# Kernel tuning notes

Measured on AMD Instinct MI355X. Metric: run time of the kernel, lower is better.

## Reference

```python
import jax, jax.numpy as jnp
import numpy as np

D_HIDDEN = 1024
N_HEADS = 16
D_HEAD = 64
B, N = 4, 1024
EPS = 1e-5


def _lin(x, w, b):
    # torch Linear: y = x @ W^T + b, w: [out, in]
    return jnp.einsum('...i,oi->...o', x, w) + b


def _ln(x, g, b):
    m = jnp.mean(x, axis=-1, keepdims=True)
    v = jnp.mean(jnp.square(x - m), axis=-1, keepdims=True)
    return (x - m) * jax.lax.rsqrt(v + EPS) * g + b


def setup_inputs() -> dict:
    key = jax.random.key(0)
    ks = jax.random.split(key, 20)
    d = D_HIDDEN
    s = 0.02
    inp = {
        'x': jax.random.normal(ks[0], (B, N, d), jnp.float32),
        'time_emb': jax.random.normal(ks[1], (B, d), jnp.float32),
        'ln1_g': jnp.ones((d,), jnp.float32),
        'ln1_b': jnp.zeros((d,), jnp.float32),
        's1_w': jax.random.normal(ks[2], (d, d), jnp.float32) * s,
        's1_b': jnp.zeros((d,), jnp.float32),
        'o1_w': jax.random.normal(ks[3], (d, d), jnp.float32) * s,
        'o1_b': jnp.zeros((d,), jnp.float32),
        'qkv_w': jax.random.normal(ks[4], (3 * d, d), jnp.float32) * s,
        'qkv_b': jnp.zeros((3 * d,), jnp.float32),
        'proj_w': jax.random.normal(ks[5], (d, d), jnp.float32) * s,
        'proj_b': jnp.zeros((d,), jnp.float32),
        'ln2_g': jnp.ones((d,), jnp.float32),
        'ln2_b': jnp.zeros((d,), jnp.float32),
        's2_w': jax.random.normal(ks[6], (d, d), jnp.float32) * s,
        's2_b': jnp.zeros((d,), jnp.float32),
        'o2_w': jax.random.normal(ks[7], (d, d), jnp.float32) * s,
        'o2_b': jnp.zeros((d,), jnp.float32),
        'up_w': jax.random.normal(ks[8], (4 * d, d), jnp.float32) * s,
        'up_b': jnp.zeros((4 * d,), jnp.float32),
        'down_w': jax.random.normal(ks[9], (d, 4 * d), jnp.float32) * s,
        'down_b': jnp.zeros((d,), jnp.float32),
    }
    return inp


def reference(x, time_emb, ln1_g, ln1_b, s1_w, s1_b, o1_w, o1_b,
              qkv_w, qkv_b, proj_w, proj_b, ln2_g, ln2_b,
              s2_w, s2_b, o2_w, o2_b, up_w, up_b, down_w, down_b):
    d = D_HIDDEN

    def ada(h, sw, sb, ow, ob):
        scale = _lin(time_emb, sw, sb)[:, None, :]   # [B,1,d]
        offset = _lin(time_emb, ow, ob)[:, None, :]
        return (1.0 + scale) * h + offset

    # attention branch
    h = ada(_ln(x, ln1_g, ln1_b), s1_w, s1_b, o1_w, o1_b)
    qkv = _lin(h, qkv_w, qkv_b)                       # [B,N,3d]
    q, k, v = jnp.split(qkv, 3, axis=-1)
    q = q.reshape(B, N, N_HEADS, D_HEAD)
    k = k.reshape(B, N, N_HEADS, D_HEAD)
    v = v.reshape(B, N, N_HEADS, D_HEAD)
    wei = jnp.einsum('bnhd,bmhd->bhnm', q, k) * (D_HEAD ** -0.5)
    wei = jax.nn.softmax(wei, axis=-1)
    attn = jnp.einsum('bhnm,bmhd->bnhd', wei, v).reshape(B, N, d)
    x = x + _lin(attn, proj_w, proj_b)

    # mlp branch (torch nn.GELU default = exact erf gelu)
    h = ada(_ln(x, ln2_g, ln2_b), s2_w, s2_b, o2_w, o2_b)
    h = jax.nn.gelu(_lin(h, up_w, up_b), approximate=False)
    x = x + _lin(h, down_w, down_b)
    return x, time_emb
```

## Files before the change

kernel.cpp:

```cpp
#include <hip/hip_runtime.h>
#include <hip/hip_bf16.h>
#include <math.h>

#define DH 1024
#define BB 4
#define NN 1024
#define NH 16
#define HD 64

typedef __attribute__((ext_vector_type(8))) short bf16x8;
typedef __attribute__((ext_vector_type(4))) float f32x4;
typedef unsigned short u16;

static __device__ __forceinline__ u16 f2bf(float f) {
  __hip_bfloat16 h = __float2bfloat16(f);
  return *reinterpret_cast<u16*>(&h);
}

#define MFMA16(a, b, c) __builtin_amdgcn_mfma_f32_16x16x32_bf16(a, b, c, 0, 0, 0)
#define VMCNT(n) asm volatile("s_waitcnt vmcnt(" #n ")" ::: "memory")
#define MEMFENCE asm volatile("" ::: "memory")

static __device__ __forceinline__ void async16(const void* g, void* l) {
  __builtin_amdgcn_global_load_lds(
      (const __attribute__((address_space(1))) void*)g,
      (__attribute__((address_space(3))) void*)l, 16, 0, 0);
}

__global__ void cvt_bf16_kernel(const float* __restrict__ in, u16* __restrict__ out, int n4) {
  int i = blockIdx.x * blockDim.x + threadIdx.x;
  if (i >= n4) return;
  float4 v = reinterpret_cast<const float4*>(in)[i];
  ushort4 o;
  o.x = f2bf(v.x); o.y = f2bf(v.y); o.z = f2bf(v.z); o.w = f2bf(v.w);
  reinterpret_cast<ushort4*>(out)[i] = o;
}

__global__ __launch_bounds__(256) void adaln_kernel(
    const float* __restrict__ e,
    const float* __restrict__ w_s1, const float* __restrict__ b_s1,
    const float* __restrict__ w_o1, const float* __restrict__ b_o1,
    const float* __restrict__ w_s2, const float* __restrict__ b_s2,
    const float* __restrict__ w_o2, const float* __restrict__ b_o2,
    float* __restrict__ out) {
  int tid = threadIdx.x, wid = tid >> 6, lane = tid & 63;
  int mat = blockIdx.y;
  const float* w; const float* bs; float addc;
  if (mat == 0)      { w = w_s1; bs = b_s1; addc = 1.f; }
  else if (mat == 1) { w = w_o1; bs = b_o1; addc = 0.f; }
  else if (mat == 2) { w = w_s2; bs = b_s2; addc = 1.f; }
  else               { w = w_o2; bs = b_o2; addc = 0.f; }
  int col = blockIdx.x * 4 + wid;
  float a0 = 0.f, a1 = 0.f, a2 = 0.f, a3 = 0.f;
  const float* wc_ = w + (size_t)col * DH;
  for (int i = 0; i < 16; ++i) {
    int k = i * 64 + lane;
    float wv = wc_[k];
    a0 += wv * e[k];
    a1 += wv * e[DH + k];
    a2 += wv * e[2 * DH + k];
    a3 += wv * e[3 * DH + k];
  }
  #pragma unroll
  for (int msk = 32; msk; msk >>= 1) {
    a0 += __shfl_xor(a0, msk); a1 += __shfl_xor(a1, msk);
    a2 += __shfl_xor(a2, msk); a3 += __shfl_xor(a3, msk);
  }
  if (lane == 0) {
    float bb = bs[col] + addc;
    out[mat * (4 * DH) + 0 * DH + col] = a0 + bb;
    out[mat * (4 * DH) + 1 * DH + col] = a1 + bb;
    out[mat * (4 * DH) + 2 * DH + col] = a2 + bb;
    out[mat * (4 * DH) + 3 * DH + col] = a3 + bb;
  }
}

__global__ __launch_bounds__(256) void ln_mod_kernel(
    const float* __restrict__ x, const float* __restrict__ g, const float* __restrict__ bta,
    const float* __restrict__ sp, const float* __restrict__ off, u16* __restrict__ out) {
  int row = blockIdx.x;
  int b = row >> 10;
  int tid = threadIdx.x;
  int wid = tid >> 6, lane = tid & 63;
  const float4 xv = reinterpret_cast<const float4*>(x + (size_t)row * DH)[tid];
  float s = xv.x + xv.y + xv.z + xv.w;
  float ss = xv.x * xv.x + xv.y * xv.y + xv.z * xv.z + xv.w * xv.w;
  #pragma unroll
  for (int m = 32; m; m >>= 1) { s += __shfl_xor(s, m); ss += __shfl_xor(ss, m); }
  __shared__ float red[8];
  if (lane == 0) { red[wid] = s; red[4 + wid] = ss; }
  __syncthreads();
  s = red[0] + red[1] + red[2] + red[3];
  ss = red[4] + red[5] + red[6] + red[7];
  float mean = s * (1.f / DH);
  float var = ss * (1.f / DH) - mean * mean;
  float rstd = rsqrtf(var + 1e-5f);
  int c = tid * 4;
  const float* spb = sp + b * DH + c;
  const float* offb = off + b * DH + c;
  float y0 = (xv.x - mean) * rstd * g[c + 0] + bta[c + 0];
  float y1 = (xv.y - mean) * rstd * g[c + 1] + bta[c + 1];
  float y2 = (xv.z - mean) * rstd * g[c + 2] + bta[c + 2];
  float y3 = (xv.w - mean) * rstd * g[c + 3] + bta[c + 3];
  ushort4 o;
  o.x = f2bf(spb[0] * y0 + offb[0]);
  o.y = f2bf(spb[1] * y1 + offb[1]);
  o.z = f2bf(spb[2] * y2 + offb[2]);
  o.w = f2bf(spb[3] * y3 + offb[3]);
  reinterpret_cast<ushort4*>(out + (size_t)row * DH)[tid] = o;
}

enum { EPI_BF16 = 0, EPI_GELU = 1, EPI_F32PART = 2 };

template <int EPI>
__global__ __launch_bounds__(512, 2) void gemm256_kernel(
    const u16* __restrict__ A, const u16* __restrict__ W,
    const float* __restrict__ bias, void* __restrict__ outp,
    int N, int K, int KT) {
  extern __shared__ u16 lds[];
  u16* Ab = lds;
  u16* Bb = lds + 32768;
  int tid = threadIdx.x;
  int wid = tid >> 6, lane = tid & 63;
  int l15 = lane & 15, l4 = lane >> 4;
  int wr = wid >> 2, wc = wid & 3;

  int nwg = gridDim.x * gridDim.y;
  int lin = blockIdx.y * gridDim.x + blockIdx.x;
  int q8 = nwg >> 3;
  int lin2 = (lin & 7) * q8 + (lin >> 3);
  int bx = lin2 % gridDim.x, by = lin2 / gridDim.x;
  int m0 = by * 256, n0 = bx * 256;
  int k0 = blockIdx.z * (KT << 5);

  f32x4 acc[8][4] = {};

  const u16* Abase = A + (size_t)m0 * K + k0;
  const u16* Wbase = W + (size_t)n0 * K + k0;
  int i0 = tid, i1 = 512 + tid;
  int r0 = i0 >> 2, c0 = (i0 & 3) ^ ((r0 >> 1) & 3);
  int r1 = i1 >> 2, c1 = (i1 & 3) ^ ((r1 >> 1) & 3);
  size_t gO0 = (size_t)r0 * K + c0 * 8;
  size_t gO1 = (size_t)r1 * K + c1 * 8;
  int lb0 = (wid * 64) * 8;
  int lb1 = (512 + wid * 64) * 8;

  auto stage = [&](int tt) {
    int q = (tt & 3) * 8192;
    const u16* Ak = Abase + tt * 32;
    const u16* Wk = Wbase + tt * 32;
    async16(Ak + gO0, &Ab[q + lb0]);
    async16(Ak + gO1, &Ab[q + lb1]);
    async16(Wk + gO0, &Bb[q + lb0]);
    async16(Wk + gO1, &Bb[q + lb1]);
  };

  auto compute = [&](int tt) {
    int q = (tt & 3) * 8192;
    bf16x8 af[8], bfr[4];
    #pragma unroll
    for (int m = 0; m < 8; ++m) {
      int row = wr * 128 + m * 16 + l15;
      int ps = l4 ^ ((row >> 1) & 3);
      af[m] = *reinterpret_cast<const bf16x8*>(&Ab[q + row * 32 + ps * 8]);
    }
    #pragma unroll
    for (int n = 0; n < 4; ++n) {
      int row = wc * 64 + n * 16 + l15;
      int ps = l4 ^ ((row >> 1) & 3);
      bfr[n] = *reinterpret_cast<const bf16x8*>(&Bb[q + row * 32 + ps * 8]);
    }
    #pragma unroll
    for (int m = 0; m < 8; ++m)
      #pragma unroll
      for (int n = 0; n < 4; ++n)
        acc[m][n] = MFMA16(af[m], bfr[n], acc[m][n]);
  };

  stage(0);
  if (KT > 1) stage(1);
  if (KT > 2) stage(2);
  for (int t = 0; t < KT; ++t) {
    if (t < KT - 3) { stage(t + 3); VMCNT(12); }
    else if (t == KT - 3) { VMCNT(8); }
    else if (t == KT - 2) { VMCNT(4); }
    else { VMCNT(0); }
    __builtin_amdgcn_s_barrier();
    MEMFENCE;
    compute(t);
    MEMFENCE;
    __builtin_amdgcn_s_barrier();
  }

  int M = gridDim.y * 256;
  float* fout = (float*)outp + (size_t)blockIdx.z * M * N;
  #pragma unroll
  for (int n = 0; n < 4; ++n) {
    int col = n0 + wc * 64 + n * 16 + l15;
    float bv = (EPI == EPI_F32PART) ? 0.f : bias[col];
    #pragma unroll
    for (int m = 0; m < 8; ++m) {
      #pragma unroll
      for (int r = 0; r < 4; ++r) {
        int rowg = m0 + wr * 128 + m * 16 + l4 * 4 + r;
        float v = acc[m][n][r] + bv;
        if (EPI == EPI_GELU) {
          v = 0.5f * v * (1.f + erff(v * 0.70710678118f));
          ((u16*)outp)[(size_t)rowg * N + col] = f2bf(v);
        } else if (EPI == EPI_BF16) {
          ((u16*)outp)[(size_t)rowg * N + col] = f2bf(v);
        } else {
          fout[(size_t)rowg * N + col] = v;
        }
      }
    }
  }
}

enum { OEPI_BF16 = 0, OEPI_GELU = 1, OEPI_RES = 2 };

template <int EPI>
__global__ __launch_bounds__(256, 3) void gemm_bt_kernel(
    const u16* __restrict__ A, const u16* __restrict__ W,
    const float* __restrict__ bias, const float* __restrict__ resid,
    void* __restrict__ outp, int N, int K) {
  __shared__ __align__(16) u16 As[2][128 * 32];
  __shared__ __align__(16) u16 Ws[2][128 * 32];
  int tid = threadIdx.x;
  int wid = tid >> 6, lane = tid & 63;
  int l15 = lane & 15, l4 = lane >> 4;
  int m0 = blockIdx.y * 128, n0 = blockIdx.x * 128;
  int wr = wid >> 1, wc = wid & 1;
  f32x4 acc[4][4] = {};

  const int KT = K >> 5;
  int idx0 = tid, idx1 = 256 + tid;
  int rowA0 = idx0 >> 2, gs0 = (idx0 & 3) ^ ((rowA0 >> 1) & 3);
  int rowA1 = idx1 >> 2, gs1 = (idx1 & 3) ^ ((rowA1 >> 1) & 3);
  const u16* Abase = A + (size_t)m0 * K;
  const u16* Wbase = W + (size_t)n0 * K;
  int lb0 = (wid * 64) * 8;
  int lb1 = (256 + wid * 64) * 8;

  auto stage = [&](int buf, int kt) {
    const u16* Ak = Abase + kt * 32;
    const u16* Wk = Wbase + kt * 32;
    async16(Ak + (size_t)rowA0 * K + gs0 * 8, &As[buf][lb0]);
    async16(Wk + (size_t)rowA0 * K + gs0 * 8, &Ws[buf][lb0]);
    async16(Ak + (size_t)rowA1 * K + gs1 * 8, &As[buf][lb1]);
    async16(Wk + (size_t)rowA1 * K + gs1 * 8, &Ws[buf][lb1]);
  };

  auto compute = [&](int buf) {
    bf16x8 af[4], wf[4];
    #pragma unroll
    for (int m = 0; m < 4; ++m) {
      int row = wr * 64 + m * 16 + l15;
      int ps = l4 ^ ((row >> 1) & 3);
      af[m] = *reinterpret_cast<const bf16x8*>(&As[buf][row * 32 + ps * 8]);
    }
    #pragma unroll
    for (int n = 0; n < 4; ++n) {
      int row = wc * 64 + n * 16 + l15;
      int ps = l4 ^ ((row >> 1) & 3);
      wf[n] = *reinterpret_cast<const bf16x8*>(&Ws[buf][row * 32 + ps * 8]);
    }
    #pragma unroll
    for (int m = 0; m < 4; ++m)
      #pragma unroll
      for (int n = 0; n < 4; ++n)
        acc[m][n] = MFMA16(af[m], wf[n], acc[m][n]);
  };

  stage(0, 0);
  __syncthreads();
  int buf = 0;
  for (int kt = 0; kt < KT - 1; ++kt) {
    stage(buf ^ 1, kt + 1);
    compute(buf);
    __syncthreads();
    buf ^= 1;
  }
  compute(buf);

  #pragma unroll
  for (int n = 0; n < 4; ++n) {
    int col = n0 + wc * 64 + n * 16 + l15;
    float bv = bias[col];
    #pragma unroll
    for (int m = 0; m < 4; ++m) {
      #pragma unroll
      for (int r = 0; r < 4; ++r) {
        int rowg = m0 + wr * 64 + m * 16 + l4 * 4 + r;
        float v = acc[m][n][r] + bv;
        if (EPI == OEPI_GELU) {
          v = 0.5f * v * (1.f + erff(v * 0.70710678118f));
          ((u16*)outp)[(size_t)rowg * N + col] = f2bf(v);
        } else if (EPI == OEPI_BF16) {
          ((u16*)outp)[(size_t)rowg * N + col] = f2bf(v);
        } else {
          ((float*)outp)[(size_t)rowg * N + col] = v + resid[(size_t)rowg * N + col];
        }
      }
    }
  }
}

__global__ __launch_bounds__(256) void reduce4_kernel(
    const float* __restrict__ part, const float* __restrict__ x2,
    const float* __restrict__ bias, float* __restrict__ out) {
  size_t i = (size_t)blockIdx.x * 256 + threadIdx.x;
  const size_t MN4 = (size_t)4096 * 1024 / 4;
  float4 a0 = reinterpret_cast<const float4*>(part)[i];
  float4 a1 = reinterpret_cast<const float4*>(part)[i + MN4];
  float4 a2 = reinterpret_cast<const float4*>(part)[i + 2 * MN4];
  float4 a3 = reinterpret_cast<const float4*>(part)[i + 3 * MN4];
  float4 xr = reinterpret_cast<const float4*>(x2)[i];
  int col = (int)((i * 4) & 1023);
  float4 bv = *reinterpret_cast<const float4*>(&bias[col]);
  float4 o;
  o.x = xr.x + bv.x + a0.x + a1.x + a2.x + a3.x;
  o.y = xr.y + bv.y + a0.y + a1.y + a2.y + a3.y;
  o.z = xr.z + bv.z + a0.z + a1.z + a2.z + a3.z;
  o.w = xr.w + bv.w + a0.w + a1.w + a2.w + a3.w;
  reinterpret_cast<float4*>(out)[i] = o;
}

__global__ __launch_bounds__(256, 4) void attn_kernel(
    const u16* __restrict__ qkv, u16* __restrict__ out) {
  __shared__ __align__(16) u16 Ks[64 * 64];
  __shared__ __align__(16) u16 Vt[64 * 64];
  __shared__ __align__(16) u16 Ps[4][16 * 64];
  int tid = threadIdx.x, wid = tid >> 6, lane = tid & 63;
  int l15 = lane & 15, l4 = lane >> 4;
  int qt = blockIdx.x, bh = blockIdx.y;
  int b = bh >> 4, h = bh & 15;
  const size_t SN = 3 * DH;
  const u16* qb = qkv + (size_t)b * NN * SN + h * HD;
  const u16* kb = qb + DH;
  const u16* vb = qb + 2 * DH;

  int qrow = qt * 64 + wid * 16 + l15;
  bf16x8 qf[2];
  #pragma unroll
  for (int ks = 0; ks < 2; ++ks)
    qf[ks] = *reinterpret_cast<const bf16x8*>(qb + (size_t)qrow * SN + ks * 32 + l4 * 8);

  float m_[4], l_[4];
  f32x4 o_[4] = {};
  #pragma unroll
  for (int r = 0; r < 4; ++r) { m_[r] = -1e30f; l_[r] = 0.f; }

  int idxA = tid, idxB = 256 + tid;
  int jA = idxA >> 3, sA = idxA & 7, gsA = sA ^ (jA & 7);
  int jB = idxB >> 3, sB = idxB & 7, gsB = sB ^ (jB & 7);
  int lbA = (wid * 64) * 8;
  int lbB = (256 + wid * 64) * 8;

  for (int t = 0; t < 16; ++t) {
    __syncthreads();
    const u16* ktb = kb + (size_t)t * 64 * SN;
    async16(ktb + (size_t)jA * SN + gsA * 8, &Ks[lbA]);
    async16(ktb + (size_t)jB * SN + gsB * 8, &Ks[lbB]);
    const u16* vtb = vb + (size_t)t * 64 * SN;
    {
      bf16x8 v0 = *reinterpret_cast<const bf16x8*>(vtb + (size_t)jA * SN + sA * 8);
      bf16x8 v1 = *reinterpret_cast<const bf16x8*>(vtb + (size_t)jB * SN + sB * 8);
      #pragma unroll
      for (int e = 0; e < 8; ++e) {
        int d = sA * 8 + e;
        int ps = (jA >> 3) ^ (d & 7) ^ ((d >> 3) & 7);
        Vt[d * 64 + ps * 8 + (jA & 7)] = v0[e];
        int d2 = sB * 8 + e;
        int ps2 = (jB >> 3) ^ (d2 & 7) ^ ((d2 >> 3) & 7);
        Vt[d2 * 64 + ps2 * 8 + (jB & 7)] = v1[e];
      }
    }
    __syncthreads();

    f32x4 sa[4];
    #pragma unroll
    for (int nb = 0; nb < 4; ++nb) {
      f32x4 s = {};
      #pragma unroll
      for (int ks = 0; ks < 2; ++ks) {
        int j = nb * 16 + l15;
        int ps = (ks * 4 + l4) ^ (j & 7);
        bf16x8 kf = *reinterpret_cast<const bf16x8*>(&Ks[j * 64 + ps * 8]);
        s = MFMA16(qf[ks], kf, s);
      }
      sa[nb] = s * 0.125f;
    }

    float corr[4], tsum[4];
    #pragma unroll
    for (int r = 0; r < 4; ++r) {
      float v = fmaxf(fmaxf(sa[0][r], sa[1][r]), fmaxf(sa[2][r], sa[3][r]));
      #pragma unroll
      for (int msk = 1; msk < 16; msk <<= 1) v = fmaxf(v, __shfl_xor(v, msk));
      float mn = fmaxf(m_[r], v);
      corr[r] = __expf(m_[r] - mn);
      m_[r] = mn;
      tsum[r] = 0.f;
    }
    #pragma unroll
    for (int nb = 0; nb < 4; ++nb) {
      #pragma unroll
      for (int r = 0; r < 4; ++r) {
        float p = __expf(sa[nb][r] - m_[r]);
        sa[nb][r] = p;
        tsum[r] += p;
      }
    }
    #pragma unroll
    for (int r = 0; r < 4; ++r) {
      float v = tsum[r];
      #pragma unroll
      for (int msk = 1; msk < 16; msk <<= 1) v += __shfl_xor(v, msk);
      l_[r] = l_[r] * corr[r] + v;
    }
    #pragma unroll
    for (int nd = 0; nd < 4; ++nd) {
      #pragma unroll
      for (int r = 0; r < 4; ++r) o_[nd][r] *= corr[r];
    }

    u16* Pw = Ps[wid];
    #pragma unroll
    for (int nb = 0; nb < 4; ++nb) {
      int slot = nb * 2 + (l15 >> 3);
      #pragma unroll
      for (int r = 0; r < 4; ++r) {
        int row = l4 * 4 + r;
        int ps = slot ^ (row & 7);
        Pw[row * 64 + ps * 8 + (l15 & 7)] = f2bf(sa[nb][r]);
      }
    }
    #pragma unroll
    for (int ks = 0; ks < 2; ++ks) {
      int psp = (ks * 4 + l4) ^ (l15 & 7);
      bf16x8 pa = *reinterpret_cast<const bf16x8*>(&Pw[l15 * 64 + psp * 8]);
      #pragma unroll
      for (int nd = 0; nd < 4; ++nd) {
        int d = nd * 16 + l15;
        int psv = (ks * 4 + l4) ^ (d & 7) ^ ((d >> 3) & 7);
        bf16x8 vf = *reinterpret_cast<const bf16x8*>(&Vt[d * 64 + psv * 8]);
        o_[nd] = MFMA16(pa, vf, o_[nd]);
      }
    }
  }

  float inv[4];
  #pragma unroll
  for (int r = 0; r < 4; ++r) inv[r] = 1.f / l_[r];
  u16* ob = out + (size_t)b * NN * DH + h * HD;
  #pragma unroll
  for (int nd = 0; nd < 4; ++nd) {
    #pragma unroll
    for (int r = 0; r < 4; ++r) {
      int q = qt * 64 + wid * 16 + l4 * 4 + r;
      ob[(size_t)q * DH + nd * 16 + l15] = f2bf(o_[nd][r] * inv[r]);
    }
  }
}

__global__ void copy_te_kernel(const float* __restrict__ te, float* __restrict__ out) {
  int i = blockIdx.x * blockDim.x + threadIdx.x;
  if (i < BB * DH) out[i] = te[i];
}

extern "C" void kernel_launch(void* const* d_in, const int* in_sizes, int n_in,
                              void* d_out, int out_size, void* d_ws, size_t ws_size,
                              hipStream_t stream) {
  (void)in_sizes; (void)n_in; (void)out_size; (void)ws_size;
  const float* x      = (const float*)d_in[0];
  const float* te     = (const float*)d_in[1];
  const float* ln1_g  = (const float*)d_in[2];
  const float* ln1_b  = (const float*)d_in[3];
  const float* s1_w   = (const float*)d_in[4];
  const float* s1_b   = (const float*)d_in[5];
  const float* o1_w   = (const float*)d_in[6];
  const float* o1_b   = (const float*)d_in[7];
  const float* qkv_w  = (const float*)d_in[8];
  const float* qkv_b  = (const float*)d_in[9];
  const float* proj_w = (const float*)d_in[10];
  const float* proj_b = (const float*)d_in[11];
  const float* ln2_g  = (const float*)d_in[12];
  const float* ln2_b  = (const float*)d_in[13];
  const float* s2_w   = (const float*)d_in[14];
  const float* s2_b   = (const float*)d_in[15];
  const float* o2_w   = (const float*)d_in[16];
  const float* o2_b   = (const float*)d_in[17];
  const float* up_w   = (const float*)d_in[18];
  const float* up_b   = (const float*)d_in[19];
  const float* down_w = (const float*)d_in[20];
  const float* down_b = (const float*)d_in[21];

  char* ws = (char*)d_ws;
  size_t off = 0;
  auto alloc = [&](size_t bytes) { void* p = ws + off; off += (bytes + 255) & ~255ull; return p; };
  u16*   wq   = (u16*)  alloc((size_t)3072 * 1024 * 2);
  u16*   wp   = (u16*)  alloc((size_t)1024 * 1024 * 2);
  u16*   wu   = (u16*)  alloc((size_t)4096 * 1024 * 2);
  u16*   h1   = (u16*)  alloc((size_t)4096 * 1024 * 2);
  u16*   qkvb = (u16*)  alloc((size_t)4096 * 3072 * 2);
  u16*   att  = (u16*)  alloc((size_t)4096 * 1024 * 2);
  u16*   h2   = (u16*)  alloc((size_t)4096 * 1024 * 2);
  u16*   wd   = (u16*)  alloc((size_t)1024 * 4096 * 2);
  float* x2   = (float*)alloc((size_t)4096 * 1024 * 4);
  u16*   upb  = (u16*)  alloc((size_t)4096 * 4096 * 2);
  float* ada  = (float*)alloc((size_t)4 * 4 * 1024 * 4);
  float* sp1 = ada, *off1 = ada + 4096, *sp2 = ada + 8192, *off2 = ada + 12288;
  float* part = (float*)wq;

  cvt_bf16_kernel<<<(3072 * 1024 / 4 + 255) / 256, 256, 0, stream>>>(qkv_w, wq, 3072 * 1024 / 4);
  cvt_bf16_kernel<<<(1024 * 1024 / 4 + 255) / 256, 256, 0, stream>>>(proj_w, wp, 1024 * 1024 / 4);
  cvt_bf16_kernel<<<(4096 * 1024 / 4 + 255) / 256, 256, 0, stream>>>(up_w, wu, 4096 * 1024 / 4);
  cvt_bf16_kernel<<<(4096 * 1024 / 4 + 255) / 256, 256, 0, stream>>>(down_w, wd, 4096 * 1024 / 4);
  adaln_kernel<<<dim3(256, 4), 256, 0, stream>>>(te, s1_w, s1_b, o1_w, o1_b, s2_w, s2_b, o2_w, o2_b, ada);
  ln_mod_kernel<<<4096, 256, 0, stream>>>(x, ln1_g, ln1_b, sp1, off1, h1);
  gemm256_kernel<EPI_BF16><<<dim3(12, 16, 1), 512, 131072, stream>>>(h1, wq, qkv_b, qkvb, 3072, 1024, 32);
  attn_kernel<<<dim3(16, 64), 256, 0, stream>>>(qkvb, att);
  gemm_bt_kernel<OEPI_RES><<<dim3(8, 32), 256, 0, stream>>>(att, wp, proj_b, x, x2, 1024, 1024);
  ln_mod_kernel<<<4096, 256, 0, stream>>>(x2, ln2_g, ln2_b, sp2, off2, h2);
  gemm256_kernel<EPI_GELU><<<dim3(16, 16, 1), 512, 131072, stream>>>(h2, wu, up_b, upb, 4096, 1024, 32);
  gemm256_kernel<EPI_F32PART><<<dim3(4, 16, 4), 512, 131072, stream>>>(upb, wd, nullptr, part, 1024, 4096, 32);
  reduce4_kernel<<<4096, 256, 0, stream>>>(part, x2, down_b, (float*)d_out);
  copy_te_kernel<<<16, 256, 0, stream>>>(te, (float*)d_out + 4096 * 1024);
}
```

Baseline: 282.7 us.

## Double-buffer K/V tiles in attention, remap blocks, and fuse weight conversions

The attention kernel now double-buffers K and V tiles in shared memory. The next tile's loads are issued before the current tile's QK/PV math, and the V transpose-write happens after the MFMAs, so each iteration needs one barrier instead of two. Block indices are remapped so neighbouring blocks share (batch, head) groups for better L2 reuse, and s_setprio raises wave priority around the PV MFMAs. The four weight-conversion launches are merged into one kernel to cut launch overhead. The double buffers double K/V LDS use, which may reduce occupancy.

Result: faster. 277.1 us (-2.0%).

```diff
diff --git a/kernel.cpp b/kernel.cpp
--- a/kernel.cpp
+++ b/kernel.cpp
@@ -27,13 +27,20 @@
       (__attribute__((address_space(3))) void*)l, 16, 0, 0);
 }
 
-__global__ void cvt_bf16_kernel(const float* __restrict__ in, u16* __restrict__ out, int n4) {
-  int i = blockIdx.x * blockDim.x + threadIdx.x;
-  if (i >= n4) return;
-  float4 v = reinterpret_cast<const float4*>(in)[i];
+__global__ void cvt_all_kernel(const float* __restrict__ wq, const float* __restrict__ wp,
+                               const float* __restrict__ wu, const float* __restrict__ wd,
+                               u16* __restrict__ oq, u16* __restrict__ op,
+                               u16* __restrict__ ou, u16* __restrict__ od) {
+  int i = blockIdx.x * 256 + threadIdx.x;
+  const float* src; u16* dst; int off;
+  if (i < 786432)            { src = wq; dst = oq; off = i; }
+  else if (i < 1048576)      { src = wp; dst = op; off = i - 786432; }
+  else if (i < 2097152)      { src = wu; dst = ou; off = i - 1048576; }
+  else                       { src = wd; dst = od; off = i - 2097152; }
+  float4 v = reinterpret_cast<const float4*>(src)[off];
   ushort4 o;
   o.x = f2bf(v.x); o.y = f2bf(v.y); o.z = f2bf(v.z); o.w = f2bf(v.w);
-  reinterpret_cast<ushort4*>(out)[i] = o;
+  reinterpret_cast<ushort4*>(dst)[off] = o;
 }
 
 __global__ __launch_bounds__(256) void adaln_kernel(
@@ -328,12 +335,14 @@
 
 __global__ __launch_bounds__(256, 4) void attn_kernel(
     const u16* __restrict__ qkv, u16* __restrict__ out) {
-  __shared__ __align__(16) u16 Ks[64 * 64];
-  __shared__ __align__(16) u16 Vt[64 * 64];
-  __shared__ __align__(16) u16 Ps[4][16 * 64];
+  __shared__ __align__(16) u16 Ks[2][4096];
+  __shared__ __align__(16) u16 Vt[2][4096];
+  __shared__ __align__(16) u16 Ps[4][1024];
   int tid = threadIdx.x, wid = tid >> 6, lane = tid & 63;
   int l15 = lane & 15, l4 = lane >> 4;
-  int qt = blockIdx.x, bh = blockIdx.y;
+  int L = blockIdx.y * gridDim.x + blockIdx.x;
+  int qt = (L >> 3) & 15;
+  int bh = (L & 7) | ((L >> 7) << 3);
   int b = bh >> 4, h = bh & 15;
   const size_t SN = 3 * DH;
   const u16* qb = qkv + (size_t)b * NN * SN + h * HD;
@@ -351,32 +360,42 @@
   #pragma unroll
   for (int r = 0; r < 4; ++r) { m_[r] = -1e30f; l_[r] = 0.f; }
 
-  int idxA = tid, idxB = 256 + tid;
-  int jA = idxA >> 3, sA = idxA & 7, gsA = sA ^ (jA & 7);
-  int jB = idxB >> 3, sB = idxB & 7, gsB = sB ^ (jB & 7);
-  int lbA = (wid * 64) * 8;
-  int lbB = (256 + wid * 64) * 8;
-
+  int iA = tid, iB = 256 + tid;
+  int jA = iA >> 3, sA = iA & 7, gsA = sA ^ (jA & 7);
+  int jB = iB >> 3, sB = iB & 7, gsB = sB ^ (jB & 7);
+
+  auto vwrite = [&](int bufn, bf16x8 v0, bf16x8 v1) {
+    #pragma unroll
+    for (int e = 0; e < 8; ++e) {
+      int d = sA * 8 + e;
+      int ps = (jA >> 3) ^ (d & 7) ^ ((d >> 3) & 7);
+      Vt[bufn][d * 64 + ps * 8 + (jA & 7)] = v0[e];
+      int d2 = sB * 8 + e;
+      int ps2 = (jB >> 3) ^ (d2 & 7) ^ ((d2 >> 3) & 7);
+      Vt[bufn][d2 * 64 + ps2 * 8 + (jB & 7)] = v1[e];
+    }
+  };
+
+  {
+    async16(kb + (size_t)jA * SN + gsA * 8, &Ks[0][iA * 8]);
+    async16(kb + (size_t)jB * SN + gsB * 8, &Ks[0][iB * 8]);
+    bf16x8 v0 = *reinterpret_cast<const bf16x8*>(vb + (size_t)jA * SN + sA * 8);
+    bf16x8 v1 = *reinterpret_cast<const bf16x8*>(vb + (size_t)jB * SN + sB * 8);
+    vwrite(0, v0, v1);
+    __syncthreads();
+  }
+
+  int buf = 0;
   for (int t = 0; t < 16; ++t) {
-    __syncthreads();
-    const u16* ktb = kb + (size_t)t * 64 * SN;
-    async16(ktb + (size_t)jA * SN + gsA * 8, &Ks[lbA]);
-    async16(ktb + (size_t)jB * SN + gsB * 8, &Ks[lbB]);
-    const u16* vtb = vb + (size_t)t * 64 * SN;
-    {
-      bf16x8 v0 = *reinterpret_cast<const bf16x8*>(vtb + (size_t)jA * SN + sA * 8);
-      bf16x8 v1 = *reinterpret_cast<const bf16x8*>(vtb + (size_t)jB * SN + sB * 8);
-      #pragma unroll
-      for (int e = 0; e < 8; ++e) {
-        int d = sA * 8 + e;
-        int ps = (jA >> 3) ^ (d & 7) ^ ((d >> 3) & 7);
-        Vt[d * 64 + ps * 8 + (jA & 7)] = v0[e];
-        int d2 = sB * 8 + e;
-        int ps2 = (jB >> 3) ^ (d2 & 7) ^ ((d2 >> 3) & 7);
-        Vt[d2 * 64 + ps2 * 8 + (jB & 7)] = v1[e];
-      }
-    }
-    __syncthreads();
+    bf16x8 vna, vnb;
+    if (t < 15) {
+      const u16* kt = kb + (size_t)(t + 1) * 64 * SN;
+      const u16* vt = vb + (size_t)(t + 1) * 64 * SN;
+      async16(kt + (size_t)jA * SN + gsA * 8, &Ks[buf ^ 1][iA * 8]);
+      async16(kt + (size_t)jB * SN + gsB * 8, &Ks[buf ^ 1][iB * 8]);
+      vna = *reinterpret_cast<const bf16x8*>(vt + (size_t)jA * SN + sA * 8);
+      vnb = *reinterpret_cast<const bf16x8*>(vt + (size_t)jB * SN + sB * 8);
+    }
 
     f32x4 sa[4];
     #pragma unroll
@@ -386,7 +405,7 @@
       for (int ks = 0; ks < 2; ++ks) {
         int j = nb * 16 + l15;
         int ps = (ks * 4 + l4) ^ (j & 7);
-        bf16x8 kf = *reinterpret_cast<const bf16x8*>(&Ks[j * 64 + ps * 8]);
+        bf16x8 kf = *reinterpret_cast<const bf16x8*>(&Ks[buf][j * 64 + ps * 8]);
         s = MFMA16(qf[ks], kf, s);
       }
       sa[nb] = s * 0.125f;
@@ -436,6 +455,8 @@
         Pw[row * 64 + ps * 8 + (l15 & 7)] = f2bf(sa[nb][r]);
       }
     }
+
+    __builtin_amdgcn_s_setprio(1);
     #pragma unroll
     for (int ks = 0; ks < 2; ++ks) {
       int psp = (ks * 4 + l4) ^ (l15 & 7);
@@ -444,10 +465,17 @@
       for (int nd = 0; nd < 4; ++nd) {
         int d = nd * 16 + l15;
         int psv = (ks * 4 + l4) ^ (d & 7) ^ ((d >> 3) & 7);
-        bf16x8 vf = *reinterpret_cast<const bf16x8*>(&Vt[d * 64 + psv * 8]);
+        bf16x8 vf = *reinterpret_cast<const bf16x8*>(&Vt[buf][d * 64 + psv * 8]);
         o_[nd] = MFMA16(pa, vf, o_[nd]);
       }
     }
+    __builtin_amdgcn_s_setprio(0);
+
+    if (t < 15) {
+      vwrite(buf ^ 1, vna, vnb);
+      __syncthreads();
+    }
+    buf ^= 1;
   }
 
   float inv[4];
@@ -513,10 +541,7 @@
   float* sp1 = ada, *off1 = ada + 4096, *sp2 = ada + 8192, *off2 = ada + 12288;
   float* part = (float*)wq;
 
-  cvt_bf16_kernel<<<(3072 * 1024 / 4 + 255) / 256, 256, 0, stream>>>(qkv_w, wq, 3072 * 1024 / 4);
-  cvt_bf16_kernel<<<(1024 * 1024 / 4 + 255) / 256, 256, 0, stream>>>(proj_w, wp, 1024 * 1024 / 4);
-  cvt_bf16_kernel<<<(4096 * 1024 / 4 + 255) / 256, 256, 0, stream>>>(up_w, wu, 4096 * 1024 / 4);
-  cvt_bf16_kernel<<<(4096 * 1024 / 4 + 255) / 256, 256, 0, stream>>>(down_w, wd, 4096 * 1024 / 4);
+  cvt_all_kernel<<<12288, 256, 0, stream>>>(qkv_w, proj_w, up_w, down_w, wq, wp, wu, wd);
   adaln_kernel<<<dim3(256, 4), 256, 0, stream>>>(te, s1_w, s1_b, o1_w, o1_b, s2_w, s2_b, o2_w, o2_b, ada);
   ln_mod_kernel<<<4096, 256, 0, stream>>>(x, ln1_g, ln1_b, sp1, off1, h1);
   gemm256_kernel<EPI_BF16><<<dim3(12, 16, 1), 512, 131072, stream>>>(h1, wq, qkv_b, qkvb, 3072, 1024, 32);
```
